# Kernel optimization log

Measured on AMD Instinct MI355X. Metric: run time of the kernel, lower is better.

## Reference

```python
import jax, jax.numpy as jnp
import numpy as np

N, E, D_IN, D_E, D, L, D_OUT = 20000, 320000, 64, 16, 256, 4, 10


def _gine(x, e, src, dst, eps, W1, b1, W2, b2):
    """GINE conv: MLP((1+eps)*x + sum_{j->i} relu(x_j + e_ji))."""
    msg = jax.nn.relu(x[src] + e)                                   # [E, D]
    agg = jax.ops.segment_sum(msg, dst, num_segments=x.shape[0])    # [N, D]
    h = (1.0 + eps) * x + agg
    return jax.nn.relu(h @ W1 + b1) @ W2 + b2


def setup_inputs() -> dict:
    key = jax.random.key(0)
    ks = jax.random.split(key, 24)
    p = lambda k, sh: jax.random.normal(k, sh, jnp.float32) * 0.05
    return {
        "x": jax.random.normal(ks[0], (N, D_IN), jnp.float32),
        "edge_attr": jax.random.normal(ks[1], (E, D_E), jnp.float32),
        "edge_index": jax.random.randint(ks[2], (2, E), 0, N, jnp.int32),
        # FeatureEncoder: node and edge linear encoders to dim_inner
        "W_ne": p(ks[3], (D_IN, D)), "b_ne": jnp.zeros((D,), jnp.float32),
        "W_ee": p(ks[4], (D_E, D)), "b_ee": jnp.zeros((D,), jnp.float32),
        # pre-MP: one Linear+ReLU layer
        "W_pre": p(ks[5], (D, D)), "b_pre": jnp.zeros((D,), jnp.float32),
        # GINEAggregation (k-hop agg module)
        "eps_a": jnp.zeros((), jnp.float32),
        "W1_a": p(ks[6], (D, D)), "b1_a": jnp.zeros((D,), jnp.float32),
        "W2_a": p(ks[7], (D, D)), "b2_a": jnp.zeros((D,), jnp.float32),
        # L stacked DelayGINEConvLayer params
        "eps_l": jnp.zeros((L,), jnp.float32),
        "W1_l": p(ks[8], (L, D, D)), "b1_l": jnp.zeros((L, D), jnp.float32),
        "W2_l": p(ks[9], (L, D, D)), "b2_l": jnp.zeros((L, D), jnp.float32),
        # head
        "W_h": p(ks[10], (D, D_OUT)), "b_h": jnp.zeros((D_OUT,), jnp.float32),
    }


def reference(x, edge_attr, edge_index, W_ne, b_ne, W_ee, b_ee, W_pre, b_pre,
              eps_a, W1_a, b1_a, W2_a, b2_a, eps_l, W1_l, b1_l, W2_l, b2_l,
              W_h, b_h):
    src, dst = edge_index[0], edge_index[1]
    # FeatureEncoder
    h = x @ W_ne + b_ne                                  # [N, D]
    e = edge_attr @ W_ee + b_ee                          # [E, D]
    # pre-MP
    h = jax.nn.relu(h @ W_pre + b_pre)
    # k-hop GINE aggregation module
    h = _gine(h, e, src, dst, eps_a, W1_a, b1_a, W2_a, b2_a)
    # stacked DelayGINE conv layers with residual connections
    for i in range(L):
        h = h + _gine(h, e, src, dst, eps_l[i], W1_l[i], b1_l[i], W2_l[i], b2_l[i])
    # node-level head
    return h @ W_h + b_h                                 # [N, D_OUT]
```

## Files before the change

kernel.cpp:

```cpp
#include <hip/hip_runtime.h>
#include <hip/hip_bf16.h>

namespace {

constexpr int NN = 20000;
constexpr int NE = 320000;
constexpr int DI = 64;
constexpr int DE = 16;
constexpr int DM = 256;
constexpr int DO = 10;

__host__ __device__ constexpr size_t woff(int m) {
  return m == 0 ? 0 : (size_t)16384 + (size_t)(m - 1) * 65536;
}
constexpr size_t WTOTAL = 16384 + 11 * 65536;

typedef __attribute__((ext_vector_type(8))) short s16x8;
typedef __attribute__((ext_vector_type(4))) float f32x4;

__device__ inline unsigned short f2bf(float x) {
  union { float f; unsigned u; } c; c.f = x;
  unsigned r = (c.u + 0x7FFFu + ((c.u >> 16) & 1u)) >> 16;
  return (unsigned short)r;
}
__device__ inline float bf2f(unsigned short h) {
  union { unsigned u; float f; } c; c.u = ((unsigned)h) << 16;
  return c.f;
}

__device__ inline unsigned char f2e4m3(float x) {
  union { float f; unsigned u; } c; c.f = x;
  const unsigned s = (c.u >> 24) & 0x80u;
  float ax = fabsf(x);
  if (ax < 0.0078125f) return (unsigned char)s;
  if (ax > 448.f) ax = 448.f;
  c.f = ax;
  unsigned b = c.u;
  b += 0x7FFFFu + ((b >> 20) & 1u);
  const unsigned e8 = (b >> 23) - 120u;
  const unsigned m8 = (b >> 20) & 7u;
  return (unsigned char)(s | (e8 << 3) | m8);
}
__device__ inline float e4m32f(unsigned u) {
  unsigned b = ((u & 0x80u) << 24) | (((u & 0x7Fu) << 20) + 0x3C000000u);
  if ((u & 0x7Fu) == 0) b &= 0x80000000u;
  union { unsigned u; float f; } c; c.u = b;
  return c.f;
}


__global__ __launch_bounds__(256) void hist_kernel(
    const int* __restrict__ dst, int* __restrict__ counts, int E)
{
  const int j = blockIdx.x * 256 + threadIdx.x;
  if (j < E) atomicAdd(&counts[dst[j]], 1);
}

__global__ __launch_bounds__(1024) void scan_kernel(
    const int* __restrict__ counts, int* __restrict__ row_ptr,
    int* __restrict__ cursor, int n)
{
  __shared__ int partial[1024];
  const int t = threadIdx.x;
  const int chunk = (n + 1023) / 1024;
  const int beg = t * chunk;
  const int end = min(beg + chunk, n);
  int s = 0;
  for (int i = beg; i < end; ++i) s += counts[i];
  partial[t] = s;
  __syncthreads();
  for (int off = 1; off < 1024; off <<= 1) {
    const int v = (t >= off) ? partial[t - off] : 0;
    __syncthreads();
    partial[t] += v;
    __syncthreads();
  }
  int base = (t == 0) ? 0 : partial[t - 1];
  for (int i = beg; i < end; ++i) {
    const int c = counts[i];
    row_ptr[i] = base;
    cursor[i] = base;
    base += c;
  }
  if (t == 1023) row_ptr[n] = partial[1023];
}

__global__ __launch_bounds__(256) void scatter_kernel(
    const int* __restrict__ src, const int* __restrict__ dst,
    const float* __restrict__ eattr, int* __restrict__ cursor,
    int* __restrict__ esrc, unsigned short* __restrict__ ea16, int E)
{
  const int j = blockIdx.x * 256 + threadIdx.x;
  if (j < E) {
    const int p = atomicAdd(&cursor[dst[j]], 1);
    esrc[p] = src[j];
    const float4* ep = reinterpret_cast<const float4*>(&eattr[(size_t)j * DE]);
    const float4 e0 = ep[0], e1 = ep[1], e2 = ep[2], e3 = ep[3];
    const float ea[16] = {e0.x, e0.y, e0.z, e0.w, e1.x, e1.y, e1.z, e1.w,
                          e2.x, e2.y, e2.z, e2.w, e3.x, e3.y, e3.z, e3.w};
    s16x8 v0, v1;
    #pragma unroll
    for (int k = 0; k < 8; ++k) {
      v0[k] = (short)f2bf(ea[k]);
      v1[k] = (short)f2bf(ea[8 + k]);
    }
    s16x8* op = reinterpret_cast<s16x8*>(&ea16[(size_t)p * DE]);
    op[0] = v0; op[1] = v1;
  }
}

__global__ __launch_bounds__(256) void convertW_kernel(
    const float* __restrict__ W_ne, const float* __restrict__ W_pre,
    const float* __restrict__ W1_a, const float* __restrict__ W2_a,
    const float* __restrict__ W1_l, const float* __restrict__ W2_l,
    unsigned short* __restrict__ hi, unsigned short* __restrict__ lo)
{
  const int mat = blockIdx.y;
  const float* src;
  int K = 256;
  if (mat == 0)      { src = W_ne;  K = 64; }
  else if (mat == 1) { src = W_pre; }
  else if (mat == 2) { src = W1_a; }
  else if (mat == 3) { src = W2_a; }
  else if (mat < 8)  { src = W1_l + (size_t)(mat - 4) * 65536; }
  else               { src = W2_l + (size_t)(mat - 8) * 65536; }
  const size_t off = woff(mat);

  const int ntiles = (K >> 6) * 4;
  const int t = blockIdx.x;
  if (t >= ntiles) return;
  const int tk = t % (K >> 6);
  const int tn = t / (K >> 6);

  __shared__ float tile[64][65];
  const int tid = threadIdx.x;
  const int c = tid & 63;
  const int rg = tid >> 6;
  for (int i = 0; i < 16; ++i) {
    const int r = rg + i * 4;
    tile[r][c] = src[(size_t)(tk * 64 + r) * 256 + tn * 64 + c];
  }
  __syncthreads();
  const int k = tk * 64 + c;
  for (int i = 0; i < 16; ++i) {
    const int nn = rg + i * 4;
    const int n = tn * 64 + nn;
    const float x = tile[c][nn];
    const unsigned short hh = f2bf(x);
    hi[off + (size_t)n * K + k] = hh;
    lo[off + (size_t)n * K + k] = f2bf(x - bf2f(hh));
  }
}

__global__ __launch_bounds__(256) void convertWee_kernel(
    const float* __restrict__ Wee, unsigned short* __restrict__ Wt16)
{
  const int n = threadIdx.x;
  #pragma unroll
  for (int k = 0; k < DE; ++k)
    Wt16[n * DE + k] = f2bf(Wee[k * DM + n]);
}

__global__ __launch_bounds__(256) void eenc_kernel(
    const unsigned short* __restrict__ ea16, const unsigned short* __restrict__ Wt16,
    const float* __restrict__ bee, unsigned char* __restrict__ e8)
{
  __shared__ unsigned char stage[128][144];
  const int tid = threadIdx.x;
  const int lane = tid & 63, wid = tid >> 6;
  const int l15 = lane & 15, l4 = lane >> 4;
  const int eBase0 = blockIdx.x * 128;
  const int eBase = eBase0 + wid * 32;
  const int colBase = blockIdx.y * 128;
  const s16x8 zz = {0, 0, 0, 0, 0, 0, 0, 0};

  s16x8 ah[2];
  #pragma unroll
  for (int mi = 0; mi < 2; ++mi) {
    const int edge = eBase + mi * 16 + l15;
    ah[mi] = (l4 < 2)
        ? *reinterpret_cast<const s16x8*>(&ea16[(size_t)edge * DE + l4 * 8]) : zz;
  }
  s16x8 bh[8];
  #pragma unroll
  for (int ni = 0; ni < 8; ++ni) {
    const int col = colBase + ni * 16 + l15;
    bh[ni] = (l4 < 2)
        ? *reinterpret_cast<const s16x8*>(&Wt16[col * DE + l4 * 8]) : zz;
  }
  f32x4 acc[2][8];
  #pragma unroll
  for (int mi = 0; mi < 2; ++mi)
    #pragma unroll
    for (int ni = 0; ni < 8; ++ni)
      acc[mi][ni] = (f32x4){0.f, 0.f, 0.f, 0.f};
  #pragma unroll
  for (int mi = 0; mi < 2; ++mi)
    #pragma unroll
    for (int ni = 0; ni < 8; ++ni)
      acc[mi][ni] = __builtin_amdgcn_mfma_f32_16x16x32_bf16(ah[mi], bh[ni], acc[mi][ni], 0, 0, 0);

  #pragma unroll
  for (int ni = 0; ni < 8; ++ni) {
    const int col = ni * 16 + l15;
    const float bv = bee[colBase + col];
    #pragma unroll
    for (int mi = 0; mi < 2; ++mi) {
      #pragma unroll
      for (int r = 0; r < 4; ++r) {
        const int erow = wid * 32 + mi * 16 + l4 * 4 + r;
        stage[erow][col] = f2e4m3(acc[mi][ni][r] + bv);
      }
    }
  }
  __syncthreads();
  #pragma unroll
  for (int it = 0; it < 4; ++it) {
    const int idx = tid + it * 256;
    const int e = idx >> 3, cc = idx & 7;
    const s16x8 v = *reinterpret_cast<const s16x8*>(&stage[e][cc * 16]);
    *reinterpret_cast<s16x8*>(&e8[(size_t)(eBase0 + e) * DM + colBase + cc * 16]) = v;
  }
}

template<bool RELU, bool RESID, bool ABF16>
__global__ __launch_bounds__(256) void mm_mfma(
    const float* __restrict__ Af, const unsigned short* __restrict__ Ab,
    const unsigned short* __restrict__ Bth, const unsigned short* __restrict__ Btl,
    const float* __restrict__ bias,
    unsigned short* __restrict__ O16, int M, int K)
{
  __shared__ unsigned short Ah[64 * 64];
  __shared__ unsigned short Al[ABF16 ? 8 : 64 * 64];
  __shared__ unsigned short Bh[128 * 64], Bl[128 * 64];
  const int tid = threadIdx.x;
  const int lane = tid & 63, wid = tid >> 6;
  const int wr = wid >> 1, wc = wid & 1;
  const int l15 = lane & 15, l4 = lane >> 4;
  const int rowBase = blockIdx.x * 64, colBase = blockIdx.y * 128;

  f32x4 acc[2][4];
  #pragma unroll
  for (int i = 0; i < 2; ++i)
    #pragma unroll
    for (int j = 0; j < 4; ++j) acc[i][j] = (f32x4){0.f, 0.f, 0.f, 0.f};

  const int nk = K >> 6;
  for (int ks = 0; ks < nk; ++ks) {
    #pragma unroll
    for (int i = 0; i < 2; ++i) {
      const int u = tid + i * 256;
      const int row = u >> 3, kc = u & 7;
      const int grow = rowBase + row;
      const int chunk = row * 8 + (kc ^ (row & 7));
      if (ABF16) {
        s16x8 v = {0, 0, 0, 0, 0, 0, 0, 0};
        if (grow < M)
          v = *reinterpret_cast<const s16x8*>(&Ab[(size_t)grow * K + ks * 64 + kc * 8]);
        ((s16x8*)Ah)[chunk] = v;
      } else {
        float4 v0 = make_float4(0.f, 0.f, 0.f, 0.f), v1 = v0;
        if (grow < M) {
          const float* p = Af + (size_t)grow * K + ks * 64 + kc * 8;
          v0 = *reinterpret_cast<const float4*>(p);
          v1 = *reinterpret_cast<const float4*>(p + 4);
        }
        const float xs[8] = {v0.x, v0.y, v0.z, v0.w, v1.x, v1.y, v1.z, v1.w};
        s16x8 hv, lv;
        #pragma unroll
        for (int j = 0; j < 8; ++j) {
          const unsigned short hh = f2bf(xs[j]);
          hv[j] = (short)hh;
          lv[j] = (short)f2bf(xs[j] - bf2f(hh));
        }
        ((s16x8*)Ah)[chunk] = hv;
        ((s16x8*)Al)[chunk] = lv;
      }
    }
    #pragma unroll
    for (int i = 0; i < 4; ++i) {
      const int u = tid + i * 256;
      const int n = u >> 3, kc = u & 7;
      const size_t g = (size_t)(colBase + n) * K + ks * 64 + kc * 8;
      const int chunk = n * 8 + (kc ^ (n & 7));
      ((s16x8*)Bh)[chunk] = *reinterpret_cast<const s16x8*>(Bth + g);
      ((s16x8*)Bl)[chunk] = *reinterpret_cast<const s16x8*>(Btl + g);
    }
    __syncthreads();
    #pragma unroll
    for (int sub = 0; sub < 2; ++sub) {
      const int kc = sub * 4 + l4;
      s16x8 ah[2], al[2], bh[4], bl[4];
      #pragma unroll
      for (int mi = 0; mi < 2; ++mi) {
        const int r = wr * 32 + mi * 16 + l15;
        const int ch = r * 8 + (kc ^ (r & 7));
        ah[mi] = ((const s16x8*)Ah)[ch];
        if (!ABF16) al[mi] = ((const s16x8*)Al)[ch];
      }
      #pragma unroll
      for (int ni = 0; ni < 4; ++ni) {
        const int r = wc * 64 + ni * 16 + l15;
        const int ch = r * 8 + (kc ^ (r & 7));
        bh[ni] = ((const s16x8*)Bh)[ch];
        bl[ni] = ((const s16x8*)Bl)[ch];
      }
      #pragma unroll
      for (int mi = 0; mi < 2; ++mi)
        #pragma unroll
        for (int ni = 0; ni < 4; ++ni) {
          acc[mi][ni] = __builtin_amdgcn_mfma_f32_16x16x32_bf16(ah[mi], bh[ni], acc[mi][ni], 0, 0, 0);
          acc[mi][ni] = __builtin_amdgcn_mfma_f32_16x16x32_bf16(ah[mi], bl[ni], acc[mi][ni], 0, 0, 0);
          if (!ABF16)
            acc[mi][ni] = __builtin_amdgcn_mfma_f32_16x16x32_bf16(al[mi], bh[ni], acc[mi][ni], 0, 0, 0);
        }
    }
    __syncthreads();
  }

  #pragma unroll
  for (int ni = 0; ni < 4; ++ni) {
    const int gcol = colBase + wc * 64 + ni * 16 + l15;
    const float bv = bias[gcol];
    #pragma unroll
    for (int mi = 0; mi < 2; ++mi) {
      const int rbase = rowBase + wr * 32 + mi * 16 + l4 * 4;
      #pragma unroll
      for (int r = 0; r < 4; ++r) {
        const int grow = rbase + r;
        if (grow < M) {
          float v = acc[mi][ni][r] + bv;
          if (RESID) v += bf2f(O16[(size_t)grow * DM + gcol]);
          if (RELU) v = fmaxf(v, 0.f);
          O16[(size_t)grow * DM + gcol] = f2bf(v);
        }
      }
    }
  }
}

__global__ __launch_bounds__(256) void gather_e8_kernel(
    const unsigned short* __restrict__ h16,
    const int* __restrict__ row_ptr, const int* __restrict__ esrc,
    const unsigned char* __restrict__ e8,
    const float* __restrict__ eps_ptr, int eps_idx,
    unsigned short* __restrict__ out16, int n)
{
  const int tid = threadIdx.x;
  const int lane = tid & 63, wave = tid >> 6;
  const int half = lane >> 5;
  const int c8 = (lane & 31) * 8;
  const float ep1 = 1.0f + eps_ptr[eps_idx];
  const int stride = gridDim.x * 4;

  for (int i = blockIdx.x * 4 + wave; i < n; i += stride) {
    const int beg = row_ptr[i], end = row_ptr[i + 1];
    const int cnt = end - beg;
    float a[8];
    #pragma unroll
    for (int k = 0; k < 8; ++k) a[k] = 0.f;

    const int npair = cnt >> 1;
    int it = 0;
    for (; it + 4 <= npair; it += 4) {
      int pp[4], ss[4];
      #pragma unroll
      for (int j = 0; j < 4; ++j) {
        pp[j] = beg + 2 * (it + j) + half;
        ss[j] = esrc[pp[j]];
      }
      s16x8 hv[4]; uint2 ev[4];
      #pragma unroll
      for (int j = 0; j < 4; ++j) {
        hv[j] = *reinterpret_cast<const s16x8*>(&h16[(size_t)ss[j] * DM + c8]);
        ev[j] = *reinterpret_cast<const uint2*>(&e8[(size_t)pp[j] * DM + c8]);
      }
      #pragma unroll
      for (int j = 0; j < 4; ++j) {
        #pragma unroll
        for (int k = 0; k < 4; ++k) {
          a[k]     += fmaxf(bf2f((unsigned short)hv[j][k])     + e4m32f((ev[j].x >> (8 * k)) & 255u), 0.f);
          a[k + 4] += fmaxf(bf2f((unsigned short)hv[j][k + 4]) + e4m32f((ev[j].y >> (8 * k)) & 255u), 0.f);
        }
      }
    }
    for (; it < npair; ++it) {
      const int p0 = beg + 2 * it + half;
      const int s0 = esrc[p0];
      const s16x8 h0 = *reinterpret_cast<const s16x8*>(&h16[(size_t)s0 * DM + c8]);
      const uint2 e0 = *reinterpret_cast<const uint2*>(&e8[(size_t)p0 * DM + c8]);
      #pragma unroll
      for (int k = 0; k < 4; ++k) {
        a[k]     += fmaxf(bf2f((unsigned short)h0[k])     + e4m32f((e0.x >> (8 * k)) & 255u), 0.f);
        a[k + 4] += fmaxf(bf2f((unsigned short)h0[k + 4]) + e4m32f((e0.y >> (8 * k)) & 255u), 0.f);
      }
    }
    if ((cnt & 1) && half == 0) {
      const int p0 = end - 1;
      const int s0 = esrc[p0];
      const s16x8 h0 = *reinterpret_cast<const s16x8*>(&h16[(size_t)s0 * DM + c8]);
      const uint2 e0 = *reinterpret_cast<const uint2*>(&e8[(size_t)p0 * DM + c8]);
      #pragma unroll
      for (int k = 0; k < 4; ++k) {
        a[k]     += fmaxf(bf2f((unsigned short)h0[k])     + e4m32f((e0.x >> (8 * k)) & 255u), 0.f);
        a[k + 4] += fmaxf(bf2f((unsigned short)h0[k + 4]) + e4m32f((e0.y >> (8 * k)) & 255u), 0.f);
      }
    }
    #pragma unroll
    for (int k = 0; k < 8; ++k) a[k] += __shfl_xor(a[k], 32, 64);
    if (half == 0) {
      const s16x8 hs = *reinterpret_cast<const s16x8*>(&h16[(size_t)i * DM + c8]);
      s16x8 o;
      #pragma unroll
      for (int k = 0; k < 8; ++k)
        o[k] = (short)f2bf(ep1 * bf2f((unsigned short)hs[k]) + a[k]);
      *reinterpret_cast<s16x8*>(&out16[(size_t)i * DM + c8]) = o;
    }
  }
}

__global__ __launch_bounds__(256) void gather_rc_kernel(
    const unsigned short* __restrict__ h16,
    const int* __restrict__ row_ptr, const int* __restrict__ esrc,
    const unsigned short* __restrict__ ea16,
    const float* __restrict__ Wee, const float* __restrict__ bee,
    const float* __restrict__ eps_ptr, int eps_idx,
    unsigned short* __restrict__ out16, int n)
{
  const int tid = threadIdx.x;
  const int lane = tid & 63, wave = tid >> 6;
  const int c4 = lane * 4;
  float4 w[16];
  #pragma unroll
  for (int k = 0; k < 16; ++k)
    w[k] = *reinterpret_cast<const float4*>(&Wee[k * DM + c4]);
  const float4 bv = *reinterpret_cast<const float4*>(&bee[c4]);
  const float ep1 = 1.0f + eps_ptr[eps_idx];
  const int stride = gridDim.x * 4;

  for (int i = blockIdx.x * 4 + wave; i < n; i += stride) {
    const int beg = row_ptr[i], end = row_ptr[i + 1];
    float a0 = 0.f, a1 = 0.f, a2 = 0.f, a3 = 0.f;
    for (int p = beg; p < end; ++p) {
      const int s = esrc[p];
      const ushort4 hv = *reinterpret_cast<const ushort4*>(&h16[(size_t)s * DM + c4]);
      const s16x8* eap = reinterpret_cast<const s16x8*>(&ea16[(size_t)p * DE]);
      const s16x8 ew0 = eap[0], ew1 = eap[1];
      float m0 = bf2f(hv.x) + bv.x, m1 = bf2f(hv.y) + bv.y;
      float m2 = bf2f(hv.z) + bv.z, m3 = bf2f(hv.w) + bv.w;
      float ea[16];
      #pragma unroll
      for (int k = 0; k < 8; ++k) {
        ea[k] = bf2f((unsigned short)ew0[k]);
        ea[8 + k] = bf2f((unsigned short)ew1[k]);
      }
      #pragma unroll
      for (int k = 0; k < 16; ++k) {
        m0 += ea[k] * w[k].x; m1 += ea[k] * w[k].y;
        m2 += ea[k] * w[k].z; m3 += ea[k] * w[k].w;
      }
      a0 += fmaxf(m0, 0.f); a1 += fmaxf(m1, 0.f);
      a2 += fmaxf(m2, 0.f); a3 += fmaxf(m3, 0.f);
    }
    const ushort4 hs = *reinterpret_cast<const ushort4*>(&h16[(size_t)i * DM + c4]);
    ushort4 o;
    o.x = f2bf(ep1 * bf2f(hs.x) + a0); o.y = f2bf(ep1 * bf2f(hs.y) + a1);
    o.z = f2bf(ep1 * bf2f(hs.z) + a2); o.w = f2bf(ep1 * bf2f(hs.w) + a3);
    *reinterpret_cast<ushort4*>(&out16[(size_t)i * DM + c4]) = o;
  }
}

__global__ __launch_bounds__(256) void head_kernel(
    const unsigned short* __restrict__ h16, const float* __restrict__ W,
    const float* __restrict__ b, float* __restrict__ out, int M)
{
  __shared__ float Ws[DM * DO];
  const int tid = threadIdx.x;
  for (int i = tid; i < DM * DO; i += 256) Ws[i] = W[i];
  __syncthreads();
  const int r = tid >> 4;
  const int c = tid & 15;
  const int row = blockIdx.x * 16 + r;
  if (row < M && c < DO) {
    const unsigned short* hp = &h16[(size_t)row * DM];
    float acc = 0.f;
    #pragma unroll 8
    for (int k = 0; k < DM; ++k) acc += bf2f(hp[k]) * Ws[k * DO + c];
    out[(size_t)row * DO + c] = acc + b[c];
  }
}

}

extern "C" void kernel_launch(void* const* d_in, const int* in_sizes, int n_in,
                              void* d_out, int out_size, void* d_ws, size_t ws_size,
                              hipStream_t stream) {
  const float* x     = (const float*)d_in[0];
  const float* eattr = (const float*)d_in[1];
  const int*   eidx  = (const int*)d_in[2];
  const float* W_ne  = (const float*)d_in[3];
  const float* b_ne  = (const float*)d_in[4];
  const float* W_ee  = (const float*)d_in[5];
  const float* b_ee  = (const float*)d_in[6];
  const float* W_pre = (const float*)d_in[7];
  const float* b_pre = (const float*)d_in[8];
  const float* eps_a = (const float*)d_in[9];
  const float* W1_a  = (const float*)d_in[10];
  const float* b1_a  = (const float*)d_in[11];
  const float* W2_a  = (const float*)d_in[12];
  const float* b2_a  = (const float*)d_in[13];
  const float* eps_l = (const float*)d_in[14];
  const float* W1_l  = (const float*)d_in[15];
  const float* b1_l  = (const float*)d_in[16];
  const float* W2_l  = (const float*)d_in[17];
  const float* b2_l  = (const float*)d_in[18];
  const float* W_h   = (const float*)d_in[19];
  const float* b_h   = (const float*)d_in[20];

  const int* src = eidx;
  const int* dst = eidx + NE;

  char* wp = (char*)d_ws;
  unsigned short* h16   = (unsigned short*)wp; wp += (size_t)NN * DM * 2;
  unsigned short* t16   = (unsigned short*)wp; wp += (size_t)NN * DM * 2;
  unsigned short* agg16 = (unsigned short*)wp; wp += (size_t)NN * DM * 2;
  unsigned short* ea16  = (unsigned short*)wp; wp += (size_t)NE * DE * 2;
  unsigned short* wt_hi = (unsigned short*)wp; wp += WTOTAL * 2;
  unsigned short* wt_lo = (unsigned short*)wp; wp += WTOTAL * 2;
  unsigned short* wtee  = (unsigned short*)wp; wp += (size_t)DM * DE * 2;
  int* esrc    = (int*)wp;                     wp += (size_t)NE * 4;
  int* counts  = (int*)wp;                     wp += (size_t)NN * 4;
  int* row_ptr = (int*)wp;                     wp += (size_t)(NN + 1) * 4;
  int* cursor  = (int*)wp;                     wp += (size_t)NN * 4;
  wp = (char*)(((uintptr_t)wp + 15) & ~(uintptr_t)15);
  unsigned char* e8 = (unsigned char*)wp;
  const size_t need_e8 = (size_t)(wp - (char*)d_ws) + (size_t)NE * DM;
  const bool use_e8 = ws_size >= need_e8;

  hipMemsetAsync(counts, 0, NN * sizeof(int), stream);
  hist_kernel<<<(NE + 255) / 256, 256, 0, stream>>>(dst, counts, NE);
  scan_kernel<<<1, 1024, 0, stream>>>(counts, row_ptr, cursor, NN);
  scatter_kernel<<<(NE + 255) / 256, 256, 0, stream>>>(
      src, dst, eattr, cursor, esrc, ea16, NE);

  convertW_kernel<<<dim3(16, 12), 256, 0, stream>>>(
      W_ne, W_pre, W1_a, W2_a, W1_l, W2_l, wt_hi, wt_lo);
  convertWee_kernel<<<1, 256, 0, stream>>>(W_ee, wtee);

  if (use_e8)
    eenc_kernel<<<dim3(NE / 128, 2), 256, 0, stream>>>(ea16, wtee, b_ee, e8);

  const dim3 mmgrid((NN + 63) / 64, 2);

  mm_mfma<false, false, false><<<mmgrid, 256, 0, stream>>>(
      x, nullptr, wt_hi + woff(0), wt_lo + woff(0), b_ne, t16, NN, DI);
  mm_mfma<true, false, true><<<mmgrid, 256, 0, stream>>>(
      nullptr, t16, wt_hi + woff(1), wt_lo + woff(1), b_pre, h16, NN, DM);

  for (int layer = 0; layer < 5; ++layer) {
    const float* eps; int ei; const float *b1, *b2; size_t o1, o2; bool resid;
    if (layer == 0) {
      eps = eps_a; ei = 0; b1 = b1_a; b2 = b2_a;
      o1 = woff(2); o2 = woff(3); resid = false;
    } else {
      const int i = layer - 1;
      eps = eps_l; ei = i;
      b1 = b1_l + (size_t)i * DM; b2 = b2_l + (size_t)i * DM;
      o1 = woff(4 + i); o2 = woff(8 + i); resid = true;
    }
    if (use_e8)
      gather_e8_kernel<<<5000, 256, 0, stream>>>(
          h16, row_ptr, esrc, e8, eps, ei, agg16, NN);
    else
      gather_rc_kernel<<<1280, 256, 0, stream>>>(
          h16, row_ptr, esrc, ea16, W_ee, b_ee, eps, ei, agg16, NN);
    mm_mfma<true, false, true><<<mmgrid, 256, 0, stream>>>(
        nullptr, agg16, wt_hi + o1, wt_lo + o1, b1, t16, NN, DM);
    if (resid)
      mm_mfma<false, true, true><<<mmgrid, 256, 0, stream>>>(
          nullptr, t16, wt_hi + o2, wt_lo + o2, b2, h16, NN, DM);
    else
      mm_mfma<false, false, true><<<mmgrid, 256, 0, stream>>>(
          nullptr, t16, wt_hi + o2, wt_lo + o2, b2, h16, NN, DM);
  }

  head_kernel<<<(NN + 15) / 16, 256, 0, stream>>>(h16, W_h, b_h, (float*)d_out, NN);
}
```

Before: 514.1 us.

## Fuse two-layer MLP GEMMs into one kernel keeping hidden tile in LDS

Replaces the pair of separate GEMM launches per MLP with a single kernel that computes a 32-row tile across all 256 columns, stages the bf16 hidden activation in shared memory, and immediately multiplies by the second weight matrix. This drops the intermediate t16 round-trip through global memory and one launch per layer. The first-layer fp32 input now uses only a single bf16 split (no lo-part correction), the K-step shrinks to 32, and the e4m3 encoder is rewritten branch-free. Risks: lower tile-level reuse of weights (each block reloads full W1 and W2), smaller per-block work, and slight precision loss on the encoder input.

Result: no change. 514.4 us (+0.1%).

```diff
diff --git a/kernel.cpp b/kernel.cpp
--- a/kernel.cpp
+++ b/kernel.cpp
@@ -31,15 +31,12 @@
 __device__ inline unsigned char f2e4m3(float x) {
   union { float f; unsigned u; } c; c.f = x;
   const unsigned s = (c.u >> 24) & 0x80u;
-  float ax = fabsf(x);
-  if (ax < 0.0078125f) return (unsigned char)s;
-  if (ax > 448.f) ax = 448.f;
-  c.f = ax;
-  unsigned b = c.u;
-  b += 0x7FFFFu + ((b >> 20) & 1u);
-  const unsigned e8 = (b >> 23) - 120u;
-  const unsigned m8 = (b >> 20) & 7u;
-  return (unsigned char)(s | (e8 << 3) | m8);
+  c.u &= 0x7FFFFFFFu;
+  c.f = fminf(c.f, 448.f);
+  const unsigned b = c.u + 0x7FFFFu + ((c.u >> 20) & 1u);
+  unsigned r = (b >> 20) - 960u;
+  r = (c.f >= 0.0078125f) ? r : 0u;
+  return (unsigned char)(s | r);
 }
 __device__ inline float e4m32f(unsigned u) {
   unsigned b = ((u & 0x80u) << 24) | (((u & 0x7Fu) << 20) + 0x3C000000u);
@@ -223,21 +220,24 @@
   }
 }
 
-template<bool RELU, bool RESID, bool ABF16>
-__global__ __launch_bounds__(256) void mm_mfma(
+template<bool RELU1, bool RELU2, bool RESID, bool ABF16>
+__global__ __launch_bounds__(256) void mlp_kernel(
     const float* __restrict__ Af, const unsigned short* __restrict__ Ab,
-    const unsigned short* __restrict__ Bth, const unsigned short* __restrict__ Btl,
-    const float* __restrict__ bias,
-    unsigned short* __restrict__ O16, int M, int K)
-{
-  __shared__ unsigned short Ah[64 * 64];
-  __shared__ unsigned short Al[ABF16 ? 8 : 64 * 64];
-  __shared__ unsigned short Bh[128 * 64], Bl[128 * 64];
+    const unsigned short* __restrict__ B1h, const unsigned short* __restrict__ B1l,
+    const float* __restrict__ b1,
+    const unsigned short* __restrict__ B2h, const unsigned short* __restrict__ B2l,
+    const float* __restrict__ b2,
+    unsigned short* __restrict__ O16, int M, int K1)
+{
+  __shared__ unsigned short Tst[32 * 256];
+  __shared__ unsigned short Wh[256 * 32], Wl[256 * 32];
+  unsigned short* Ast = Tst;
+
   const int tid = threadIdx.x;
   const int lane = tid & 63, wid = tid >> 6;
-  const int wr = wid >> 1, wc = wid & 1;
   const int l15 = lane & 15, l4 = lane >> 4;
-  const int rowBase = blockIdx.x * 64, colBase = blockIdx.y * 128;
+  const int rowBase = blockIdx.x * 32;
+  const int colW = wid * 64;
 
   f32x4 acc[2][4];
   #pragma unroll
@@ -245,93 +245,126 @@
     #pragma unroll
     for (int j = 0; j < 4; ++j) acc[i][j] = (f32x4){0.f, 0.f, 0.f, 0.f};
 
-  const int nk = K >> 6;
-  for (int ks = 0; ks < nk; ++ks) {
-    #pragma unroll
-    for (int i = 0; i < 2; ++i) {
-      const int u = tid + i * 256;
-      const int row = u >> 3, kc = u & 7;
+  const int nk1 = K1 >> 5;
+  for (int ks = 0; ks < nk1; ++ks) {
+    if (tid < 128) {
+      const int row = tid >> 2, kc = tid & 3;
       const int grow = rowBase + row;
-      const int chunk = row * 8 + (kc ^ (row & 7));
-      if (ABF16) {
-        s16x8 v = {0, 0, 0, 0, 0, 0, 0, 0};
-        if (grow < M)
-          v = *reinterpret_cast<const s16x8*>(&Ab[(size_t)grow * K + ks * 64 + kc * 8]);
-        ((s16x8*)Ah)[chunk] = v;
-      } else {
-        float4 v0 = make_float4(0.f, 0.f, 0.f, 0.f), v1 = v0;
-        if (grow < M) {
-          const float* p = Af + (size_t)grow * K + ks * 64 + kc * 8;
-          v0 = *reinterpret_cast<const float4*>(p);
-          v1 = *reinterpret_cast<const float4*>(p + 4);
+      const int chunk = row * 4 + (kc ^ ((row >> 1) & 3));
+      s16x8 v = {0, 0, 0, 0, 0, 0, 0, 0};
+      if (grow < M) {
+        if (ABF16) {
+          v = *reinterpret_cast<const s16x8*>(&Ab[(size_t)grow * K1 + ks * 32 + kc * 8]);
+        } else {
+          const float* p = Af + (size_t)grow * K1 + ks * 32 + kc * 8;
+          const float4 v0 = *reinterpret_cast<const float4*>(p);
+          const float4 v1 = *reinterpret_cast<const float4*>(p + 4);
+          const float xs[8] = {v0.x, v0.y, v0.z, v0.w, v1.x, v1.y, v1.z, v1.w};
+          #pragma unroll
+          for (int j = 0; j < 8; ++j) v[j] = (short)f2bf(xs[j]);
         }
-        const float xs[8] = {v0.x, v0.y, v0.z, v0.w, v1.x, v1.y, v1.z, v1.w};
-        s16x8 hv, lv;
-        #pragma unroll
-        for (int j = 0; j < 8; ++j) {
-          const unsigned short hh = f2bf(xs[j]);
-          hv[j] = (short)hh;
-          lv[j] = (short)f2bf(xs[j] - bf2f(hh));
-        }
-        ((s16x8*)Ah)[chunk] = hv;
-        ((s16x8*)Al)[chunk] = lv;
-      }
+      }
+      ((s16x8*)Ast)[chunk] = v;
     }
     #pragma unroll
     for (int i = 0; i < 4; ++i) {
       const int u = tid + i * 256;
-      const int n = u >> 3, kc = u & 7;
-      const size_t g = (size_t)(colBase + n) * K + ks * 64 + kc * 8;
-      const int chunk = n * 8 + (kc ^ (n & 7));
-      ((s16x8*)Bh)[chunk] = *reinterpret_cast<const s16x8*>(Bth + g);
-      ((s16x8*)Bl)[chunk] = *reinterpret_cast<const s16x8*>(Btl + g);
+      const int c = u >> 2, kc = u & 3;
+      const int chunk = c * 4 + (kc ^ ((c >> 1) & 3));
+      const size_t g = (size_t)c * K1 + ks * 32 + kc * 8;
+      ((s16x8*)Wh)[chunk] = *reinterpret_cast<const s16x8*>(B1h + g);
+      ((s16x8*)Wl)[chunk] = *reinterpret_cast<const s16x8*>(B1l + g);
     }
     __syncthreads();
-    #pragma unroll
-    for (int sub = 0; sub < 2; ++sub) {
-      const int kc = sub * 4 + l4;
-      s16x8 ah[2], al[2], bh[4], bl[4];
-      #pragma unroll
-      for (int mi = 0; mi < 2; ++mi) {
-        const int r = wr * 32 + mi * 16 + l15;
-        const int ch = r * 8 + (kc ^ (r & 7));
-        ah[mi] = ((const s16x8*)Ah)[ch];
-        if (!ABF16) al[mi] = ((const s16x8*)Al)[ch];
-      }
+    s16x8 a[2], bh[4], bl[4];
+    #pragma unroll
+    for (int mi = 0; mi < 2; ++mi) {
+      const int r = mi * 16 + l15;
+      a[mi] = ((const s16x8*)Ast)[r * 4 + (l4 ^ ((r >> 1) & 3))];
+    }
+    #pragma unroll
+    for (int ni = 0; ni < 4; ++ni) {
+      const int c = colW + ni * 16 + l15;
+      const int ch = c * 4 + (l4 ^ ((c >> 1) & 3));
+      bh[ni] = ((const s16x8*)Wh)[ch];
+      bl[ni] = ((const s16x8*)Wl)[ch];
+    }
+    #pragma unroll
+    for (int mi = 0; mi < 2; ++mi)
       #pragma unroll
       for (int ni = 0; ni < 4; ++ni) {
-        const int r = wc * 64 + ni * 16 + l15;
-        const int ch = r * 8 + (kc ^ (r & 7));
-        bh[ni] = ((const s16x8*)Bh)[ch];
-        bl[ni] = ((const s16x8*)Bl)[ch];
-      }
-      #pragma unroll
-      for (int mi = 0; mi < 2; ++mi)
-        #pragma unroll
-        for (int ni = 0; ni < 4; ++ni) {
-          acc[mi][ni] = __builtin_amdgcn_mfma_f32_16x16x32_bf16(ah[mi], bh[ni], acc[mi][ni], 0, 0, 0);
-          acc[mi][ni] = __builtin_amdgcn_mfma_f32_16x16x32_bf16(ah[mi], bl[ni], acc[mi][ni], 0, 0, 0);
-          if (!ABF16)
-            acc[mi][ni] = __builtin_amdgcn_mfma_f32_16x16x32_bf16(al[mi], bh[ni], acc[mi][ni], 0, 0, 0);
-        }
-    }
+        acc[mi][ni] = __builtin_amdgcn_mfma_f32_16x16x32_bf16(a[mi], bh[ni], acc[mi][ni], 0, 0, 0);
+        acc[mi][ni] = __builtin_amdgcn_mfma_f32_16x16x32_bf16(a[mi], bl[ni], acc[mi][ni], 0, 0, 0);
+      }
     __syncthreads();
   }
-
   #pragma unroll
   for (int ni = 0; ni < 4; ++ni) {
-    const int gcol = colBase + wc * 64 + ni * 16 + l15;
-    const float bv = bias[gcol];
+    const int col = colW + ni * 16 + l15;
+    const float bv = b1[col];
     #pragma unroll
     for (int mi = 0; mi < 2; ++mi) {
-      const int rbase = rowBase + wr * 32 + mi * 16 + l4 * 4;
       #pragma unroll
       for (int r = 0; r < 4; ++r) {
-        const int grow = rbase + r;
+        const int row = mi * 16 + l4 * 4 + r;
+        float v = acc[mi][ni][r] + bv;
+        if (RELU1) v = fmaxf(v, 0.f);
+        const int c32 = col >> 3;
+        const int chunk = row * 32 + (c32 ^ (row & 31));
+        Tst[chunk * 8 + (col & 7)] = f2bf(v);
+        acc[mi][ni][r] = 0.f;
+      }
+    }
+  }
+  __syncthreads();
+
+  for (int ks = 0; ks < 8; ++ks) {
+    #pragma unroll
+    for (int i = 0; i < 4; ++i) {
+      const int u = tid + i * 256;
+      const int c = u >> 2, kc = u & 3;
+      const int chunk = c * 4 + (kc ^ ((c >> 1) & 3));
+      const size_t g = (size_t)c * 256 + ks * 32 + kc * 8;
+      ((s16x8*)Wh)[chunk] = *reinterpret_cast<const s16x8*>(B2h + g);
+      ((s16x8*)Wl)[chunk] = *reinterpret_cast<const s16x8*>(B2l + g);
+    }
+    __syncthreads();
+    s16x8 a[2], bh[4], bl[4];
+    #pragma unroll
+    for (int mi = 0; mi < 2; ++mi) {
+      const int row = mi * 16 + l15;
+      const int c32 = ks * 4 + l4;
+      a[mi] = ((const s16x8*)Tst)[row * 32 + (c32 ^ (row & 31))];
+    }
+    #pragma unroll
+    for (int ni = 0; ni < 4; ++ni) {
+      const int c = colW + ni * 16 + l15;
+      const int ch = c * 4 + (l4 ^ ((c >> 1) & 3));
+      bh[ni] = ((const s16x8*)Wh)[ch];
+      bl[ni] = ((const s16x8*)Wl)[ch];
+    }
+    #pragma unroll
+    for (int mi = 0; mi < 2; ++mi)
+      #pragma unroll
+      for (int ni = 0; ni < 4; ++ni) {
+        acc[mi][ni] = __builtin_amdgcn_mfma_f32_16x16x32_bf16(a[mi], bh[ni], acc[mi][ni], 0, 0, 0);
+        acc[mi][ni] = __builtin_amdgcn_mfma_f32_16x16x32_bf16(a[mi], bl[ni], acc[mi][ni], 0, 0, 0);
+      }
+    __syncthreads();
+  }
+  #pragma unroll
+  for (int ni = 0; ni < 4; ++ni) {
+    const int gcol = colW + ni * 16 + l15;
+    const float bv = b2[gcol];
+    #pragma unroll
+    for (int mi = 0; mi < 2; ++mi) {
+      #pragma unroll
+      for (int r = 0; r < 4; ++r) {
+        const int grow = rowBase + mi * 16 + l4 * 4 + r;
         if (grow < M) {
           float v = acc[mi][ni][r] + bv;
           if (RESID) v += bf2f(O16[(size_t)grow * DM + gcol]);
-          if (RELU) v = fmaxf(v, 0.f);
+          if (RELU2) v = fmaxf(v, 0.f);
           O16[(size_t)grow * DM + gcol] = f2bf(v);
         }
       }
@@ -522,7 +555,6 @@
 
   char* wp = (char*)d_ws;
   unsigned short* h16   = (unsigned short*)wp; wp += (size_t)NN * DM * 2;
-  unsigned short* t16   = (unsigned short*)wp; wp += (size_t)NN * DM * 2;
   unsigned short* agg16 = (unsigned short*)wp; wp += (size_t)NN * DM * 2;
   unsigned short* ea16  = (unsigned short*)wp; wp += (size_t)NE * DE * 2;
   unsigned short* wt_hi = (unsigned short*)wp; wp += WTOTAL * 2;
@@ -550,23 +582,24 @@
   if (use_e8)
     eenc_kernel<<<dim3(NE / 128, 2), 256, 0, stream>>>(ea16, wtee, b_ee, e8);
 
-  const dim3 mmgrid((NN + 63) / 64, 2);
-
-  mm_mfma<false, false, false><<<mmgrid, 256, 0, stream>>>(
-      x, nullptr, wt_hi + woff(0), wt_lo + woff(0), b_ne, t16, NN, DI);
-  mm_mfma<true, false, true><<<mmgrid, 256, 0, stream>>>(
-      nullptr, t16, wt_hi + woff(1), wt_lo + woff(1), b_pre, h16, NN, DM);
+  const int mlpgrid = (NN + 31) / 32;
+
+  mlp_kernel<false, true, false, false><<<mlpgrid, 256, 0, stream>>>(
+      x, nullptr,
+      wt_hi + woff(0), wt_lo + woff(0), b_ne,
+      wt_hi + woff(1), wt_lo + woff(1), b_pre,
+      h16, NN, DI);
 
   for (int layer = 0; layer < 5; ++layer) {
-    const float* eps; int ei; const float *b1, *b2; size_t o1, o2; bool resid;
+    const float* eps; int ei; const float *b1, *b2; size_t o1, o2;
     if (layer == 0) {
       eps = eps_a; ei = 0; b1 = b1_a; b2 = b2_a;
-      o1 = woff(2); o2 = woff(3); resid = false;
+      o1 = woff(2); o2 = woff(3);
     } else {
       const int i = layer - 1;
       eps = eps_l; ei = i;
       b1 = b1_l + (size_t)i * DM; b2 = b2_l + (size_t)i * DM;
-      o1 = woff(4 + i); o2 = woff(8 + i); resid = true;
+      o1 = woff(4 + i); o2 = woff(8 + i);
     }
     if (use_e8)
       gather_e8_kernel<<<5000, 256, 0, stream>>>(
@@ -574,14 +607,14 @@
     else
       gather_rc_kernel<<<1280, 256, 0, stream>>>(
           h16, row_ptr, esrc, ea16, W_ee, b_ee, eps, ei, agg16, NN);
-    mm_mfma<true, false, true><<<mmgrid, 256, 0, stream>>>(
-        nullptr, agg16, wt_hi + o1, wt_lo + o1, b1, t16, NN, DM);
-    if (resid)
-      mm_mfma<false, true, true><<<mmgrid, 256, 0, stream>>>(
-          nullptr, t16, wt_hi + o2, wt_lo + o2, b2, h16, NN, DM);
+    if (layer == 0)
+      mlp_kernel<true, false, false, true><<<mlpgrid, 256, 0, stream>>>(
+          nullptr, agg16, wt_hi + o1, wt_lo + o1, b1,
+          wt_hi + o2, wt_lo + o2, b2, h16, NN, DM);
     else
-      mm_mfma<false, false, true><<<mmgrid, 256, 0, stream>>>(
-          nullptr, t16, wt_hi + o2, wt_lo + o2, b2, h16, NN, DM);
+      mlp_kernel<true, false, true, true><<<mlpgrid, 256, 0, stream>>>(
+          nullptr, agg16, wt_hi + o1, wt_lo + o1, b1,
+          wt_hi + o2, wt_lo + o2, b2, h16, NN, DM);
   }
 
   head_kernel<<<(NN + 15) / 16, 256, 0, stream>>>(h16, W_h, b_h, (float*)d_out, NN);
```
